# Kernel optimization log

Hardware: AMD Instinct MI355X
Metric: run time of the kernel (lower is better)

Reference implementation:

```python
import jax, jax.numpy as jnp
import numpy as np

N0, N1, N2, N3, B = 120000, 20000, 6000, 1600, 64
E1, E2, E3 = 480000, 144000, 38400
KS = 5  # kernel size per dim; K = 125 total


def spline_basis(pseudo, ks=KS):
    # open B-spline basis, degree 1, over [0,1]^3 (torch_spline_conv semantics)
    p = pseudo * (ks - 1)                       # (E,3)
    lo = jnp.clip(jnp.floor(p), 0.0, ks - 2.0)  # (E,3)
    f = p - lo                                  # fractional part
    bits = jnp.array([[(s >> d) & 1 for d in range(3)] for s in range(8)],
                     dtype=jnp.float32)         # (8,3) corner offsets
    w = jnp.where(bits[None] > 0, f[:, None, :], 1.0 - f[:, None, :])  # (E,8,3)
    basis = w[..., 0] * w[..., 1] * w[..., 2]   # (E,8)
    strides = jnp.array([1.0, ks, ks * ks], dtype=jnp.float32)
    kidx = ((lo[:, None, :] + bits[None]) * strides).sum(-1).astype(jnp.int32)  # (E,8)
    return basis, kidx


def spline_conv(x, edge_index, pseudo, W, root, bias, num_nodes):
    src, dst = edge_index[0], edge_index[1]
    basis, kidx = spline_basis(pseudo)                   # (E,8), (E,8)
    XW = jnp.einsum('ni,kio->nko', x, W)                 # (N,K,out)
    taps = XW[src[:, None], kidx]                        # (E,8,out) gather
    msg = (taps * basis[..., None]).sum(axis=1)          # (E,out)
    agg = jax.ops.segment_sum(msg, dst, num_segments=num_nodes)
    deg = jax.ops.segment_sum(jnp.ones_like(dst, jnp.float32), dst,
                              num_segments=num_nodes)
    agg = agg / jnp.maximum(deg, 1.0)[:, None]           # mean aggregation
    return agg + x @ root + bias


def seg_max(x, seg, n):
    v = jax.ops.segment_max(x, seg, num_segments=n)
    return jnp.where(jnp.isfinite(v), v, 0.0)  # empty voxels -> 0


def setup_inputs() -> dict:
    key = jax.random.key(0)
    ks = jax.random.split(key, 24)
    return {
        'x0': jax.random.uniform(ks[0], (N0, 1), jnp.float32),
        'cluster0': jax.random.randint(ks[1], (N0,), 0, N1),
        'edge1': jax.random.randint(ks[2], (2, E1), 0, N1),
        'pseudo1': jax.random.uniform(ks[3], (E1, 3), jnp.float32),
        'W1': jax.random.normal(ks[4], (125, 1, 64), jnp.float32) * 0.1,
        'root1': jax.random.normal(ks[5], (1, 64), jnp.float32) * 0.1,
        'b1': jnp.zeros((64,), jnp.float32),
        'cluster1': jax.random.randint(ks[6], (N1,), 0, N2),
        'edge2': jax.random.randint(ks[7], (2, E2), 0, N2),
        'pseudo2': jax.random.uniform(ks[8], (E2, 3), jnp.float32),
        'W2': jax.random.normal(ks[9], (125, 64, 64), jnp.float32) * 0.05,
        'root2': jax.random.normal(ks[10], (64, 64), jnp.float32) * 0.05,
        'b2': jnp.zeros((64,), jnp.float32),
        'cluster2': jax.random.randint(ks[11], (N2,), 0, N3),
        'edge3': jax.random.randint(ks[12], (2, E3), 0, N3),
        'pseudo3': jax.random.uniform(ks[13], (E3, 3), jnp.float32),
        'W3': jax.random.normal(ks[14], (125, 64, 128), jnp.float32) * 0.05,
        'root3': jax.random.normal(ks[15], (64, 128), jnp.float32) * 0.05,
        'b3': jnp.zeros((128,), jnp.float32),
        'cluster3': jax.random.randint(ks[16], (N3,), 0, B * 8),
        'fc1_w': jax.random.normal(ks[17], (1024, 256), jnp.float32) * 0.03,
        'fc1_b': jnp.zeros((256,), jnp.float32),
        'fc2_w': jax.random.normal(ks[18], (256, 10), jnp.float32) * 0.06,
        'fc2_b': jnp.zeros((10,), jnp.float32),
    }


def reference(x0, cluster0, edge1, pseudo1, W1, root1, b1,
              cluster1, edge2, pseudo2, W2, root2, b2,
              cluster2, edge3, pseudo3, W3, root3, b3,
              cluster3, fc1_w, fc1_b, fc2_w, fc2_b):
    x = seg_max(x0, cluster0, N1)                       # sparse voxel max pool 1
    x = jax.nn.elu(spline_conv(x, edge1, pseudo1, W1, root1, b1, N1))
    x = seg_max(x, cluster1, N2)                        # pool 2
    x = jax.nn.elu(spline_conv(x, edge2, pseudo2, W2, root2, b2, N2))
    x = seg_max(x, cluster2, N3)                        # pool 3
    x = jax.nn.elu(spline_conv(x, edge3, pseudo3, W3, root3, b3, N3))
    x = seg_max(x, cluster3, B * 8)                     # dense 2x2x2 voxel pool
    x = x.reshape(B, 8 * 128)
    x = jax.nn.elu(x @ fc1_w + fc1_b)
    x = x @ fc2_w + fc2_b
    return jax.nn.log_softmax(x, axis=1)
```

## Files before the change

### kernel.cpp

```cpp
#include <hip/hip_runtime.h>
#include <hip/hip_bf16.h>
#include <math.h>

#define N0c 120000
#define N1c 20000
#define N2c 6000
#define N3c 1600
#define E1c 480000
#define E2c 144000
#define E3c 38400

#define HB1 256
#define HB2 480
#define HB3 160
#define CVT2B 2000
#define CVT3B 4000
#define SS0B  469

typedef __attribute__((ext_vector_type(8))) short short8;
typedef __attribute__((ext_vector_type(4))) float f32x4;

__device__ __forceinline__ float eluf(float x) {
    return x > 0.0f ? x : expm1f(x);
}

__device__ __forceinline__ unsigned f2sort(float f) {
    unsigned u = __float_as_uint(f);
    return (u & 0x80000000u) ? ~u : (u | 0x80000000u);
}
__device__ __forceinline__ float sort2f(unsigned u) {
    unsigned bits = (u & 0x80000000u) ? (u & 0x7FFFFFFFu) : ~u;
    return __uint_as_float(bits);
}
__device__ __forceinline__ unsigned short f2bf(float v) {
    unsigned u = __float_as_uint(v);
    unsigned r = (u + 0x7FFFu + ((u >> 16) & 1u)) >> 16;
    return (unsigned short)r;
}

__global__ __launch_bounds__(256) void hist_all(
    const int* __restrict__ edge1, const int* __restrict__ edge2,
    const int* __restrict__ edge3,
    const float* __restrict__ pseudo2, const float* __restrict__ pseudo3,
    const float* __restrict__ W2, const float* __restrict__ W3,
    const float* __restrict__ x0, const int* __restrict__ cluster0,
    int* __restrict__ blockCnt1, int* __restrict__ binTot1,
    int* __restrict__ blockCnt2, int* __restrict__ binTot2, int* __restrict__ cntD2,
    int* __restrict__ blockCnt3, int* __restrict__ binTot3, int* __restrict__ cntD3,
    unsigned short* __restrict__ W2t, unsigned short* __restrict__ W3t,
    unsigned* __restrict__ xm1)
{
    __shared__ int h[1250];
    int b = blockIdx.x, t = threadIdx.x;
    if (b < HB1) {
        for (int i = t; i < 1250; i += 256) h[i] = 0;
        __syncthreads();
        for (int e = b * 256 + t; e < E1c; e += HB1 * 256)
            atomicAdd(&h[edge1[E1c + e] >> 4], 1);
        __syncthreads();
        for (int i = t; i < 1250; i += 256) {
            int v = h[i];
            blockCnt1[i * HB1 + b] = v;
            if (v) atomicAdd(&binTot1[i], v);
        }
    } else if (b < HB1 + HB2 + HB3) {
        bool is2 = b < HB1 + HB2;
        int rb = is2 ? (b - HB1) : (b - HB1 - HB2);
        int nblk = is2 ? HB2 : HB3;
        int E = is2 ? E2c : E3c;
        const int* edge = is2 ? edge2 : edge3;
        const float* pseudo = is2 ? pseudo2 : pseudo3;
        int* blockCnt = is2 ? blockCnt2 : blockCnt3;
        int* binTot = is2 ? binTot2 : binTot3;
        int* dstCnt = is2 ? cntD2 : cntD3;
        int nb = is2 ? HB2 : HB3;
        if (t < 64) h[t] = 0;
        __syncthreads();
        for (int e = rb * 256 + t; e < E; e += nblk * 256) {
            int c = 0, mul = 1;
            #pragma unroll
            for (int d = 0; d < 3; d++) {
                float p = pseudo[e * 3 + d] * 4.0f;
                float l = fminf(fmaxf(floorf(p), 0.0f), 3.0f);
                c += (int)l * mul;
                mul <<= 2;
            }
            atomicAdd(&h[c], 1);
            atomicAdd(&dstCnt[edge[E + e]], 1);
        }
        __syncthreads();
        if (t < 64) {
            int v = h[t];
            blockCnt[t * nb + rb] = v;
            if (v) atomicAdd(&binTot[t], v);
        }
    } else if (b < HB1 + HB2 + HB3 + CVT2B) {
        int idx = (b - (HB1 + HB2 + HB3)) * 256 + t;
        if (idx < 125 * 64 * 64) {
            int ic = idx & 63, kn = idx >> 6;
            int n = kn & 63, k = kn >> 6;
            W2t[idx] = f2bf(W2[((size_t)k * 64 + ic) * 64 + n]);
        }
    } else if (b < HB1 + HB2 + HB3 + CVT2B + CVT3B) {
        int idx = (b - (HB1 + HB2 + HB3 + CVT2B)) * 256 + t;
        if (idx < 125 * 128 * 64) {
            int ic = idx & 63, kn = idx >> 6;
            int n = kn & 127, k = kn >> 7;
            W3t[idx] = f2bf(W3[((size_t)k * 64 + ic) * 128 + n]);
        }
    } else {
        int idx = (b - (HB1 + HB2 + HB3 + CVT2B + CVT3B)) * 256 + t;
        if (idx < N0c)
            atomicMax(&xm1[cluster0[idx]], f2sort(x0[idx]));
    }
}

__global__ __launch_bounds__(256) void plan_tot(
    const int* __restrict__ binTot1, int* __restrict__ start1,
    const int* __restrict__ binTot2, int* __restrict__ binCnt2,
    int* __restrict__ binStart2, int* __restrict__ blkPrefix2,
    int* __restrict__ chunkBin2, int* __restrict__ chunkOff2,
    const int* __restrict__ binTot3, int* __restrict__ binCnt3,
    int* __restrict__ binStart3, int* __restrict__ blkPrefix3,
    int* __restrict__ chunkBin3, int* __restrict__ chunkOff3,
    const int* __restrict__ cntD2, int* __restrict__ dstStart2,
    const int* __restrict__ cntD3, int* __restrict__ dstStart3)
{
    __shared__ int ps[256];
    __shared__ int ps64[64];
    int t = threadIdx.x;

    int loc[5];
    int s = 0;
    #pragma unroll
    for (int i = 0; i < 5; i++) {
        int bin = t * 5 + i;
        int v = (bin < 1250) ? binTot1[bin] : 0;
        loc[i] = v;
        s += v;
    }
    ps[t] = s;
    __syncthreads();
    for (int ofs = 1; ofs < 256; ofs <<= 1) {
        int add = (t >= ofs) ? ps[t - ofs] : 0;
        __syncthreads();
        ps[t] += add;
        __syncthreads();
    }
    int run = (t == 0) ? 0 : ps[t - 1];
    #pragma unroll
    for (int i = 0; i < 5; i++) {
        int bin = t * 5 + i;
        if (bin < 1250) {
            start1[bin] = run;
            run += loc[i];
        }
    }
    if (t == 255) start1[1250] = run;
    __syncthreads();

    if (t < 64) {
        int v = binTot2[t];
        binCnt2[t] = v;
        ps64[t] = v;
    }
    __syncthreads();
    if (t == 0) {
        int s2 = 0, p = 0;
        for (int c = 0; c < 64; c++) {
            int v = ps64[c];
            binStart2[c] = s2;
            blkPrefix2[c] = p;
            s2 += v;
            p += (v + 63) >> 6;
        }
        binStart2[64] = s2;
        blkPrefix2[64] = p;
    }
    __syncthreads();
    if (t < 64) {
        int nch = (binCnt2[t] + 63) >> 6;
        int base = blkPrefix2[t];
        for (int j = 0; j < nch; j++) {
            chunkBin2[base + j] = t;
            chunkOff2[base + j] = j;
        }
    }
    __syncthreads();

    if (t < 64) {
        int v = binTot3[t];
        binCnt3[t] = v;
        ps64[t] = v;
    }
    __syncthreads();
    if (t == 0) {
        int s3 = 0, p = 0;
        for (int c = 0; c < 64; c++) {
            int v = ps64[c];
            binStart3[c] = s3;
            blkPrefix3[c] = p;
            s3 += v;
            p += (v + 63) >> 6;
        }
        binStart3[64] = s3;
        blkPrefix3[64] = p;
    }
    __syncthreads();
    if (t < 64) {
        int nch = (binCnt3[t] + 63) >> 6;
        int base = blkPrefix3[t];
        for (int j = 0; j < nch; j++) {
            chunkBin3[base + j] = t;
            chunkOff3[base + j] = j;
        }
    }
    __syncthreads();

    {
        int locd[24];
        int sd = 0;
        #pragma unroll
        for (int i = 0; i < 24; i++) {
            int bin = t * 24 + i;
            int vv = (bin < N2c) ? cntD2[bin] : 0;
            locd[i] = vv;
            sd += vv;
        }
        ps[t] = sd;
        __syncthreads();
        for (int ofs = 1; ofs < 256; ofs <<= 1) {
            int add = (t >= ofs) ? ps[t - ofs] : 0;
            __syncthreads();
            ps[t] += add;
            __syncthreads();
        }
        int rund = (t == 0) ? 0 : ps[t - 1];
        #pragma unroll
        for (int i = 0; i < 24; i++) {
            int bin = t * 24 + i;
            if (bin < N2c) { dstStart2[bin] = rund; rund += locd[i]; }
        }
        if (t == 255) dstStart2[N2c] = ps[255];
    }
    __syncthreads();

    {
        int locd[7];
        int sd = 0;
        #pragma unroll
        for (int i = 0; i < 7; i++) {
            int bin = t * 7 + i;
            int vv = (bin < N3c) ? cntD3[bin] : 0;
            locd[i] = vv;
            sd += vv;
        }
        ps[t] = sd;
        __syncthreads();
        for (int ofs = 1; ofs < 256; ofs <<= 1) {
            int add = (t >= ofs) ? ps[t - ofs] : 0;
            __syncthreads();
            ps[t] += add;
            __syncthreads();
        }
        int rund = (t == 0) ? 0 : ps[t - 1];
        #pragma unroll
        for (int i = 0; i < 7; i++) {
            int bin = t * 7 + i;
            if (bin < N3c) { dstStart3[bin] = rund; rund += locd[i]; }
        }
        if (t == 255) dstStart3[N3c] = ps[255];
    }
}

__global__ __launch_bounds__(256) void off_all(
    const int* __restrict__ blockCnt1, const int* __restrict__ start1,
    int* __restrict__ blockOff1,
    const int* __restrict__ blockCnt2, const int* __restrict__ binStart2,
    int* __restrict__ blockOff2,
    const int* __restrict__ blockCnt3, const int* __restrict__ binStart3,
    int* __restrict__ blockOff3)
{
    int wid = (blockIdx.x * 256 + threadIdx.x) >> 6;
    int lane = threadIdx.x & 63;
    if (wid >= 1250 + 64 + 64) return;
    const int* c;
    int* o;
    int run, width;
    if (wid < 1250) {
        c = blockCnt1 + (size_t)wid * HB1;
        o = blockOff1 + (size_t)wid * HB1;
        run = start1[wid];
        width = HB1;
    } else if (wid < 1250 + 64) {
        int bin = wid - 1250;
        c = blockCnt2 + (size_t)bin * HB2;
        o = blockOff2 + (size_t)bin * HB2;
        run = binStart2[bin];
        width = HB2;
    } else {
        int bin = wid - 1314;
        c = blockCnt3 + (size_t)bin * HB3;
        o = blockOff3 + (size_t)bin * HB3;
        run = binStart3[bin];
        width = HB3;
    }
    for (int base = 0; base < width; base += 64) {
        int b = base + lane;
        int v = (b < width) ? c[b] : 0;
        int inc = v;
        #pragma unroll
        for (int ofs = 1; ofs < 64; ofs <<= 1) {
            int u = __shfl_up(inc, ofs);
            if (lane >= ofs) inc += u;
        }
        if (b < width) o[b] = run + inc - v;
        run += __shfl(inc, 63);
    }
}

__global__ __launch_bounds__(256) void scatter_all(
    const int* __restrict__ edge1, const float* __restrict__ pseudo1,
    const int* __restrict__ edge2, const float* __restrict__ pseudo2,
    const int* __restrict__ edge3, const float* __restrict__ pseudo3,
    const int* __restrict__ blockOff1, const int* __restrict__ blockOff2,
    const int* __restrict__ blockOff3,
    int4* __restrict__ rec1, int4* __restrict__ rec2, int4* __restrict__ rec3,
    unsigned* __restrict__ xm1,
    const int* __restrict__ dstStart2, const int* __restrict__ dstStart3,
    int* __restrict__ curD2, int* __restrict__ curD3,
    int* __restrict__ posList2, int* __restrict__ posList3)
{
    __shared__ int cur[1250];
    int b = blockIdx.x, t = threadIdx.x;
    if (b < HB1) {
        for (int i = t; i < 1250; i += 256) cur[i] = blockOff1[(size_t)i * HB1 + b];
        __syncthreads();
        for (int e = b * 256 + t; e < E1c; e += HB1 * 256) {
            int src = edge1[e], dst = edge1[E1c + e];
            float f[3];
            int kbase = 0, mul5 = 1;
            #pragma unroll
            for (int d = 0; d < 3; d++) {
                float pp = pseudo1[e * 3 + d] * 4.0f;
                float l = fminf(fmaxf(floorf(pp), 0.0f), 3.0f);
                f[d] = pp - l;
                kbase += (int)l * mul5;
                mul5 *= 5;
            }
            int p = atomicAdd(&cur[dst >> 4], 1);
            rec1[p] = make_int4(src | ((dst & 15) << 16) | (kbase << 20),
                                __float_as_int(f[0]), __float_as_int(f[1]),
                                __float_as_int(f[2]));
        }
    } else if (b < HB1 + HB2 + HB3) {
        bool is2 = b < HB1 + HB2;
        int rb = is2 ? (b - HB1) : (b - HB1 - HB2);
        int nblk = is2 ? HB2 : HB3;
        int E = is2 ? E2c : E3c;
        const int* edge = is2 ? edge2 : edge3;
        const float* pseudo = is2 ? pseudo2 : pseudo3;
        const int* blockOff = is2 ? blockOff2 : blockOff3;
        int4* rec = is2 ? rec2 : rec3;
        const int* dstStart = is2 ? dstStart2 : dstStart3;
        int* curD = is2 ? curD2 : curD3;
        int* posList = is2 ? posList2 : posList3;
        int nb = is2 ? HB2 : HB3;
        if (t < 64) cur[t] = blockOff[(size_t)t * nb + rb];
        __syncthreads();
        for (int e = rb * 256 + t; e < E; e += nblk * 256) {
            int src = edge[e], dst = edge[E + e];
            float f[3];
            int c = 0, mul = 1;
            #pragma unroll
            for (int d = 0; d < 3; d++) {
                float pp = pseudo[e * 3 + d] * 4.0f;
                float l = fminf(fmaxf(floorf(pp), 0.0f), 3.0f);
                f[d] = pp - l;
                c += (int)l * mul;
                mul <<= 2;
            }
            int p = atomicAdd(&cur[c], 1);
            rec[p] = make_int4(src | (dst << 16),
                               __float_as_int(f[0]), __float_as_int(f[1]),
                               __float_as_int(f[2]));
            int qd = dstStart[dst] + atomicAdd(&curD[dst], 1);
            posList[qd] = p;
        }
    } else {
        int idx = (b - (HB1 + HB2 + HB3)) * 256 + t;
        if (idx < N1c) {
            float f = sort2f(xm1[idx]);
            unsigned bb = __float_as_uint(f);
            if ((bb & 0x7F800000u) == 0x7F800000u) f = 0.0f;
            ((float*)xm1)[idx] = f;
        }
    }
}

__global__ __launch_bounds__(256) void conv1_block(
    const int4* __restrict__ rec, const float* __restrict__ x,
    const int* __restrict__ start,
    const float* __restrict__ W, const float* __restrict__ root,
    const float* __restrict__ bias, const int* __restrict__ cl,
    unsigned* __restrict__ xmOut) {
    __shared__ float T[16][128];
    __shared__ int degL[16];
    int b = blockIdx.x;
    for (int j = threadIdx.x; j < 2048; j += 256) ((float*)T)[j] = 0.0f;
    if (threadIdx.x < 16) degL[threadIdx.x] = 0;
    __syncthreads();
    int s0 = start[b], s1 = start[b + 1];
    for (int i = s0 + threadIdx.x; i < s1; i += 256) {
        int4 r = rec[i];
        int src = r.x & 0xFFFF;
        int ln = (r.x >> 16) & 15;
        int kbase = r.x >> 20;
        float f0 = __int_as_float(r.y);
        float f1 = __int_as_float(r.z);
        float f2 = __int_as_float(r.w);
        float xv = x[src];
        #pragma unroll
        for (int s = 0; s < 8; s++) {
            int b0 = s & 1, b1 = (s >> 1) & 1, b2 = (s >> 2) & 1;
            float w0 = b0 ? f0 : 1.0f - f0;
            float w1 = b1 ? f1 : 1.0f - f1;
            float w2 = b2 ? f2 : 1.0f - f2;
            int k = kbase + b0 + 5 * b1 + 25 * b2;
            atomicAdd(&T[ln][k], xv * w0 * w1 * w2);
        }
        atomicAdd(&degL[ln], 1);
    }
    __syncthreads();
    int w = threadIdx.x >> 6, lane = threadIdx.x & 63;
    float acc[4] = {0.0f, 0.0f, 0.0f, 0.0f};
    for (int k = 0; k < 125; k++) {
        float wv = W[(k << 6) + lane];
        #pragma unroll
        for (int j = 0; j < 4; j++)
            acc[j] = fmaf(T[w + 4 * j][k], wv, acc[j]);
    }
    int v0 = b << 4;
    #pragma unroll
    for (int j = 0; j < 4; j++) {
        int ln = w + 4 * j;
        int v = v0 + ln;
        float d = fmaxf((float)degL[ln], 1.0f);
        float val = eluf(acc[j] / d + x[v] * root[lane] + bias[lane]);
        atomicMax(&xmOut[((size_t)cl[v] << 6) + lane], f2sort(val));
    }
}

__global__ void decode_cvt(unsigned* __restrict__ buf,
                           unsigned short* __restrict__ xb, int total) {
    int idx = blockIdx.x * blockDim.x + threadIdx.x;
    if (idx >= total) return;
    float f = sort2f(buf[idx]);
    unsigned b = __float_as_uint(f);
    if ((b & 0x7F800000u) == 0x7F800000u) f = 0.0f;
    ((float*)buf)[idx] = f;
    xb[idx] = f2bf(f);
}

__global__ void segmax_decode(unsigned* __restrict__ buf, int total) {
    int idx = blockIdx.x * blockDim.x + threadIdx.x;
    if (idx >= total) return;
    float f = sort2f(buf[idx]);
    unsigned b = __float_as_uint(f);
    if ((b & 0x7F800000u) == 0x7F800000u) f = 0.0f;
    ((float*)buf)[idx] = f;
}

template<int COUT>
__global__ __launch_bounds__(256) void spline_mfma(
    const int4* __restrict__ recs,
    const unsigned short* __restrict__ Wt,
    const unsigned short* __restrict__ xb,
    const int* __restrict__ binStart,
    const int* __restrict__ binCnt,
    const int* __restrict__ blkPrefix,
    const int* __restrict__ chunkBin,
    const int* __restrict__ chunkOff,
    float* __restrict__ msg)
{
    __shared__ float basisS[4][8][64];
    __shared__ int srcS[4][64];

    int w = threadIdx.x >> 6, lane = threadIdx.x & 63;
    int c = blockIdx.x * 4 + w;
    if (c >= blkPrefix[64]) return;
    int bin = chunkBin[c];
    int chunk = chunkOff[c];
    int cnt = binCnt[bin];

    {
        int pos = chunk * 64 + lane;
        bool act = pos < cnt;
        int4 r = act ? recs[binStart[bin] + pos] : make_int4(0, 0, 0, 0);
        srcS[w][lane] = r.x & 0xFFFF;
        float f0 = __int_as_float(r.y);
        float f1 = __int_as_float(r.z);
        float f2 = __int_as_float(r.w);
        #pragma unroll
        for (int s = 0; s < 8; s++) {
            float w0 = (s & 1) ? f0 : 1.0f - f0;
            float w1 = (s & 2) ? f1 : 1.0f - f1;
            float w2 = (s & 4) ? f2 : 1.0f - f2;
            basisS[w][s][lane] = act ? (w0 * w1 * w2) : 0.0f;
        }
    }
    __builtin_amdgcn_wave_barrier();
    __threadfence_block();

    int lo0 = bin & 3, lo1 = (bin >> 2) & 3, lo2 = bin >> 4;
    int kbase = lo0 + 5 * lo1 + 25 * lo2;
    int colOff = (COUT == 128) ? (blockIdx.y << 6) : 0;
    int q = lane >> 4;
    int mcol = lane & 15;

    short8 afr[4][2];
    #pragma unroll
    for (int rt = 0; rt < 4; rt++) {
        int src = srcS[w][rt * 16 + mcol];
        const unsigned short* xr = xb + ((size_t)src << 6) + q * 8;
        afr[rt][0] = *(const short8*)(xr);
        afr[rt][1] = *(const short8*)(xr + 32);
    }

    f32x4 acc[4][4];
    #pragma unroll
    for (int rt = 0; rt < 4; rt++)
        #pragma unroll
        for (int nt = 0; nt < 4; nt++)
            acc[rt][nt] = (f32x4){0.0f, 0.0f, 0.0f, 0.0f};
    const f32x4 zero4 = {0.0f, 0.0f, 0.0f, 0.0f};

    #pragma unroll 1
    for (int s = 0; s < 8; s++) {
        int k = kbase + (s & 1) + 5 * ((s >> 1) & 1) + 25 * (s >> 2);
        const unsigned short* Wk = Wt + ((size_t)k * COUT + colOff) * 64;
        short8 bfr[4][2];
        #pragma unroll
        for (int nt = 0; nt < 4; nt++) {
            const unsigned short* Wn = Wk + (size_t)(nt * 16 + mcol) * 64 + q * 8;
            bfr[nt][0] = *(const short8*)(Wn);
            bfr[nt][1] = *(const short8*)(Wn + 32);
        }
        #pragma unroll
        for (int rt = 0; rt < 4; rt++) {
            f32x4 ct[4];
            #pragma unroll
            for (int nt = 0; nt < 4; nt++) {
                ct[nt] = __builtin_amdgcn_mfma_f32_16x16x32_bf16(afr[rt][0], bfr[nt][0], zero4, 0, 0, 0);
                ct[nt] = __builtin_amdgcn_mfma_f32_16x16x32_bf16(afr[rt][1], bfr[nt][1], ct[nt], 0, 0, 0);
            }
            #pragma unroll
            for (int r = 0; r < 4; r++) {
                float bs = basisS[w][s][rt * 16 + q * 4 + r];
                #pragma unroll
                for (int nt = 0; nt < 4; nt++)
                    acc[rt][nt][r] = fmaf(bs, ct[nt][r], acc[rt][nt][r]);
            }
        }
    }

    int base = binStart[bin] + chunk * 64;
    #pragma unroll
    for (int rt = 0; rt < 4; rt++) {
        #pragma unroll
        for (int r = 0; r < 4; r++) {
            int row = rt * 16 + q * 4 + r;
            if (chunk * 64 + row < cnt) {
                float* mp = msg + (size_t)(base + row) * COUT + colOff + mcol;
                #pragma unroll
                for (int nt = 0; nt < 4; nt++)
                    mp[nt * 16] = acc[rt][nt][r];
            }
        }
    }
}

__global__ __launch_bounds__(256) void agg_update64(
    const float* __restrict__ msg, const int* __restrict__ posList,
    const int* __restrict__ dstStart,
    const float* __restrict__ xm, const float* __restrict__ root,
    const float* __restrict__ bias, const int* __restrict__ cl,
    unsigned* __restrict__ xmOut, int nNodes) {
    __shared__ float xsh[4][64];
    int w = threadIdx.x >> 6, lane = threadIdx.x & 63;
    int v = blockIdx.x * 4 + w;
    if (v >= nNodes) return;
    xsh[w][lane] = xm[((size_t)v << 6) + lane];
    int s0 = dstStart[v], s1 = dstStart[v + 1];
    float a0 = 0.0f, a1 = 0.0f, a2 = 0.0f, a3 = 0.0f;
    int i = s0;
    for (; i + 4 <= s1; i += 4) {
        int p0 = posList[i], p1 = posList[i + 1];
        int p2 = posList[i + 2], p3 = posList[i + 3];
        a0 += msg[((size_t)p0 << 6) + lane];
        a1 += msg[((size_t)p1 << 6) + lane];
        a2 += msg[((size_t)p2 << 6) + lane];
        a3 += msg[((size_t)p3 << 6) + lane];
    }
    for (; i < s1; i++)
        a0 += msg[((size_t)posList[i] << 6) + lane];
    float a = (a0 + a1 + a2 + a3) / fmaxf((float)(s1 - s0), 1.0f);
    float r = 0.0f;
    #pragma unroll 8
    for (int j = 0; j < 64; j++)
        r = fmaf(xsh[w][j], root[(j << 6) + lane], r);
    float val = eluf(a + r + bias[lane]);
    atomicMax(&xmOut[((size_t)cl[v] << 6) + lane], f2sort(val));
}

__global__ __launch_bounds__(256) void agg_update128(
    const float* __restrict__ msg, const int* __restrict__ posList,
    const int* __restrict__ dstStart,
    const float* __restrict__ xm, const float* __restrict__ root,
    const float* __restrict__ bias, const int* __restrict__ cl,
    unsigned* __restrict__ xmOut, int nNodes) {
    __shared__ float xsh[4][64];
    int w = threadIdx.x >> 6, lane = threadIdx.x & 63;
    int v = blockIdx.x * 4 + w;
    if (v >= nNodes) return;
    xsh[w][lane] = xm[((size_t)v << 6) + lane];
    int s0 = dstStart[v], s1 = dstStart[v + 1];
    float c0a = 0.0f, c0b = 0.0f, c1a = 0.0f, c1b = 0.0f;
    int i = s0;
    for (; i + 2 <= s1; i += 2) {
        int p0 = posList[i], p1 = posList[i + 1];
        const float* m0 = msg + ((size_t)p0 << 7);
        const float* m1 = msg + ((size_t)p1 << 7);
        c0a += m0[lane]; c0b += m0[64 + lane];
        c1a += m1[lane]; c1b += m1[64 + lane];
    }
    for (; i < s1; i++) {
        const float* m0 = msg + ((size_t)posList[i] << 7);
        c0a += m0[lane]; c0b += m0[64 + lane];
    }
    float dinv = 1.0f / fmaxf((float)(s1 - s0), 1.0f);
    float aa0 = (c0a + c1a) * dinv;
    float aa1 = (c0b + c1b) * dinv;
    float r0 = 0.0f, r1 = 0.0f;
    #pragma unroll 8
    for (int j = 0; j < 64; j++) {
        float xi = xsh[w][j];
        r0 = fmaf(xi, root[(j << 7) + lane], r0);
        r1 = fmaf(xi, root[(j << 7) + 64 + lane], r1);
    }
    unsigned* orow = xmOut + ((size_t)cl[v] << 7);
    atomicMax(&orow[lane], f2sort(eluf(aa0 + r0 + bias[lane])));
    atomicMax(&orow[64 + lane], f2sort(eluf(aa1 + r1 + bias[lane + 64])));
}

__global__ __launch_bounds__(256) void fc1_split(
    const float* __restrict__ xin, const float* __restrict__ w1,
    float* __restrict__ h) {
    __shared__ float xsh[128];
    int row = blockIdx.x, ks = blockIdx.y;
    int o = threadIdx.x;
    if (o < 128) xsh[o] = xin[row * 1024 + ks * 128 + o];
    __syncthreads();
    float acc = 0.0f;
    const float* wp = w1 + (size_t)ks * 128 * 256 + o;
    #pragma unroll 8
    for (int i = 0; i < 128; i++)
        acc = fmaf(xsh[i], wp[i * 256], acc);
    atomicAdd(&h[row * 256 + o], acc);
}

__global__ __launch_bounds__(64) void fc2_k(
    const float* __restrict__ h, const float* __restrict__ b1,
    const float* __restrict__ w2, const float* __restrict__ b2,
    float* __restrict__ out) {
    __shared__ float hs[256];
    __shared__ float lg[10];
    int row = blockIdx.x;
    int t = threadIdx.x;
    for (int i = t; i < 256; i += 64) hs[i] = eluf(h[row * 256 + i] + b1[i]);
    __syncthreads();
    if (t < 10) {
        float a = b2[t];
        for (int i = 0; i < 256; i++) a = fmaf(hs[i], w2[i * 10 + t], a);
        lg[t] = a;
    }
    __syncthreads();
    if (t < 10) {
        float m = -1e30f;
        #pragma unroll
        for (int j = 0; j < 10; j++) m = fmaxf(m, lg[j]);
        float sum = 0.0f;
        #pragma unroll
        for (int j = 0; j < 10; j++) sum += expf(lg[j] - m);
        out[row * 10 + t] = lg[t] - m - logf(sum);
    }
}

extern "C" void kernel_launch(void* const* d_in, const int* in_sizes, int n_in,
                              void* d_out, int out_size, void* d_ws, size_t ws_size,
                              hipStream_t stream) {
    const float* x0      = (const float*)d_in[0];
    const int*   cluster0= (const int*)d_in[1];
    const int*   edge1   = (const int*)d_in[2];
    const float* pseudo1 = (const float*)d_in[3];
    const float* W1      = (const float*)d_in[4];
    const float* root1   = (const float*)d_in[5];
    const float* b1      = (const float*)d_in[6];
    const int*   cluster1= (const int*)d_in[7];
    const int*   edge2   = (const int*)d_in[8];
    const float* pseudo2 = (const float*)d_in[9];
    const float* W2      = (const float*)d_in[10];
    const float* root2   = (const float*)d_in[11];
    const float* b2      = (const float*)d_in[12];
    const int*   cluster2= (const int*)d_in[13];
    const int*   edge3   = (const int*)d_in[14];
    const float* pseudo3 = (const float*)d_in[15];
    const float* W3      = (const float*)d_in[16];
    const float* root3   = (const float*)d_in[17];
    const float* b3      = (const float*)d_in[18];
    const int*   cluster3= (const int*)d_in[19];
    const float* fc1_w   = (const float*)d_in[20];
    const float* fc1_b   = (const float*)d_in[21];
    const float* fc2_w   = (const float*)d_in[22];
    const float* fc2_b   = (const float*)d_in[23];
    float* out = (float*)d_out;

    float* ws = (float*)d_ws;
    size_t off = 0;
    float* xm1  = ws + off; off += 20480;
    float* xm2  = ws + off; off += (size_t)N2c * 64;
    float* xm3  = ws + off; off += (size_t)N3c * 64;
    float* xm4  = ws + off; off += 512 * 128;
    float* h1   = ws + off; off += 64 * 256;
    int* cntD2   = (int*)(ws + off); off += 6016;
    int* cntD3   = (int*)(ws + off); off += 1664;
    int* curD2   = (int*)(ws + off); off += 6016;
    int* curD3   = (int*)(ws + off); off += 1664;
    int* binTot1 = (int*)(ws + off); off += 1280;
    int* binTot2 = (int*)(ws + off); off += 64;
    int* binTot3 = (int*)(ws + off); off += 64;
    size_t zeroFloats = off;
    int4* rec1 = (int4*)(ws + off); off += (size_t)E1c * 4;
    int4* rec2 = (int4*)(ws + off); off += (size_t)E2c * 4;
    int4* rec3 = (int4*)(ws + off); off += (size_t)E3c * 4;
    unsigned short* W2t = (unsigned short*)(ws + off); off += 256000;
    unsigned short* W3t = (unsigned short*)(ws + off); off += 512000;
    unsigned short* xb2 = (unsigned short*)(ws + off); off += 192000;
    unsigned short* xb3 = (unsigned short*)(ws + off); off += 51200;
    int* start1    = (int*)(ws + off); off += 1280;
    int* blockCnt1 = (int*)(ws + off); off += (size_t)HB1 * 1250;
    int* blockOff1 = (int*)(ws + off); off += (size_t)HB1 * 1250;
    int* blockCnt2 = (int*)(ws + off); off += (size_t)HB2 * 64;
    int* blockOff2 = (int*)(ws + off); off += (size_t)HB2 * 64;
    int* blockCnt3 = (int*)(ws + off); off += (size_t)HB3 * 64;
    int* blockOff3 = (int*)(ws + off); off += (size_t)HB3 * 64;
    int* binCnt2   = (int*)(ws + off); off += 64;
    int* binStart2 = (int*)(ws + off); off += 80;
    int* blkPrefix2= (int*)(ws + off); off += 80;
    int* chunkBin2 = (int*)(ws + off); off += 2560;
    int* chunkOff2 = (int*)(ws + off); off += 2560;
    int* binCnt3   = (int*)(ws + off); off += 64;
    int* binStart3 = (int*)(ws + off); off += 80;
    int* blkPrefix3= (int*)(ws + off); off += 80;
    int* chunkBin3 = (int*)(ws + off); off += 768;
    int* chunkOff3 = (int*)(ws + off); off += 768;
    int* dstStart2 = (int*)(ws + off); off += 6016;
    int* dstStart3 = (int*)(ws + off); off += 1664;
    int* posList2  = (int*)(ws + off); off += E2c;
    int* posList3  = (int*)(ws + off); off += E3c;
    float* msg = ws + off; off += (size_t)E2c * 64;

    hipMemsetAsync(d_ws, 0, zeroFloats * sizeof(float), stream);

    hist_all<<<HB1 + HB2 + HB3 + CVT2B + CVT3B + SS0B, 256, 0, stream>>>(
        edge1, edge2, edge3, pseudo2, pseudo3, W2, W3, x0, cluster0,
        blockCnt1, binTot1, blockCnt2, binTot2, cntD2,
        blockCnt3, binTot3, cntD3, W2t, W3t, (unsigned*)xm1);

    plan_tot<<<1, 256, 0, stream>>>(
        binTot1, start1,
        binTot2, binCnt2, binStart2, blkPrefix2, chunkBin2, chunkOff2,
        binTot3, binCnt3, binStart3, blkPrefix3, chunkBin3, chunkOff3,
        cntD2, dstStart2, cntD3, dstStart3);

    off_all<<<(1378 * 64 + 255) / 256, 256, 0, stream>>>(
        blockCnt1, start1, blockOff1,
        blockCnt2, binStart2, blockOff2,
        blockCnt3, binStart3, blockOff3);

    scatter_all<<<HB1 + HB2 + HB3 + (N1c + 255) / 256, 256, 0, stream>>>(
        edge1, pseudo1, edge2, pseudo2, edge3, pseudo3,
        blockOff1, blockOff2, blockOff3, rec1, rec2, rec3, (unsigned*)xm1,
        dstStart2, dstStart3, curD2, curD3, posList2, posList3);

    conv1_block<<<1250, 256, 0, stream>>>(rec1, xm1, start1, W1, root1, b1,
                                          cluster1, (unsigned*)xm2);
    decode_cvt<<<(N2c * 64) / 256, 256, 0, stream>>>((unsigned*)xm2, xb2, N2c * 64);

    spline_mfma<64><<<dim3((E2c / 64 + 64 + 3) / 4, 1), 256, 0, stream>>>(
        rec2, W2t, xb2, binStart2, binCnt2, blkPrefix2, chunkBin2, chunkOff2, msg);
    agg_update64<<<(N2c + 3) / 4, 256, 0, stream>>>(msg, posList2, dstStart2,
                                                    xm2, root2, b2, cluster2,
                                                    (unsigned*)xm3, N2c);
    decode_cvt<<<(N3c * 64) / 256, 256, 0, stream>>>((unsigned*)xm3, xb3, N3c * 64);

    spline_mfma<128><<<dim3((E3c / 64 + 64 + 3) / 4, 2), 256, 0, stream>>>(
        rec3, W3t, xb3, binStart3, binCnt3, blkPrefix3, chunkBin3, chunkOff3, msg);
    agg_update128<<<(N3c + 3) / 4, 256, 0, stream>>>(msg, posList3, dstStart3,
                                                     xm3, root3, b3, cluster3,
                                                     (unsigned*)xm4, N3c);
    segmax_decode<<<(512 * 128) / 256, 256, 0, stream>>>((unsigned*)xm4, 512 * 128);

    fc1_split<<<dim3(64, 8), 256, 0, stream>>>(xm4, fc1_w, h1);
    fc2_k<<<64, 64, 0, stream>>>(h1, fc1_b, fc2_w, fc2_b, out);
}
```

Baseline: 327.0 us.

## Use per-destination CSR for conv1, fp16 messages, LDS weight transpose, fuse decode

Conv1 edge bucketing moves from per-block 1250-bin histograms plus offset tables to a per-destination count, scan and atomic-cursor scatter, which removes the blockCnt1/blockOff1 traffic and their offset pass. The in-kernel degree count is replaced by dstStart differences. Weight transposition to bf16 now goes through a padded LDS tile per kernel index instead of thousands of strided-gather blocks. Edge messages between the MFMA and aggregation kernels are stored as fp16 rather than fp32, halving that traffic at some precision cost. The final seg-max decode is folded into fc1, removing one launch. The trade-off is that the conv1 scatter now uses global atomics per destination, which may contend more than the previous shared-memory bins.

```diff
diff --git a/kernel.cpp b/kernel.cpp
--- a/kernel.cpp
+++ b/kernel.cpp
@@ -1,5 +1,6 @@
 #include <hip/hip_runtime.h>
 #include <hip/hip_bf16.h>
+#include <hip/hip_fp16.h>
 #include <math.h>
 
 #define N0c 120000
@@ -13,8 +14,7 @@
 #define HB1 256
 #define HB2 480
 #define HB3 160
-#define CVT2B 2000
-#define CVT3B 4000
+#define WCVB 125
 #define SS0B  469
 
 typedef __attribute__((ext_vector_type(8))) short short8;
@@ -36,6 +36,12 @@
     unsigned u = __float_as_uint(v);
     unsigned r = (u + 0x7FFFu + ((u >> 16) & 1u)) >> 16;
     return (unsigned short)r;
+}
+__device__ __forceinline__ unsigned short f2h(float v) {
+    return __half_as_ushort(__float2half(v));
+}
+__device__ __forceinline__ float h2f(unsigned short u) {
+    return __half2float(__ushort_as_half(u));
 }
 
 __global__ __launch_bounds__(256) void hist_all(
@@ -44,25 +50,18 @@
     const float* __restrict__ pseudo2, const float* __restrict__ pseudo3,
     const float* __restrict__ W2, const float* __restrict__ W3,
     const float* __restrict__ x0, const int* __restrict__ cluster0,
-    int* __restrict__ blockCnt1, int* __restrict__ binTot1,
+    int* __restrict__ cntD1,
     int* __restrict__ blockCnt2, int* __restrict__ binTot2, int* __restrict__ cntD2,
     int* __restrict__ blockCnt3, int* __restrict__ binTot3, int* __restrict__ cntD3,
     unsigned short* __restrict__ W2t, unsigned short* __restrict__ W3t,
     unsigned* __restrict__ xm1)
 {
-    __shared__ int h[1250];
+    __shared__ float smf[64 * 129];
+    int* h = (int*)smf;
     int b = blockIdx.x, t = threadIdx.x;
     if (b < HB1) {
-        for (int i = t; i < 1250; i += 256) h[i] = 0;
-        __syncthreads();
         for (int e = b * 256 + t; e < E1c; e += HB1 * 256)
-            atomicAdd(&h[edge1[E1c + e] >> 4], 1);
-        __syncthreads();
-        for (int i = t; i < 1250; i += 256) {
-            int v = h[i];
-            blockCnt1[i * HB1 + b] = v;
-            if (v) atomicAdd(&binTot1[i], v);
-        }
+            atomicAdd(&cntD1[edge1[E1c + e]], 1);
     } else if (b < HB1 + HB2 + HB3) {
         bool is2 = b < HB1 + HB2;
         int rb = is2 ? (b - HB1) : (b - HB1 - HB2);
@@ -94,29 +93,37 @@
             blockCnt[t * nb + rb] = v;
             if (v) atomicAdd(&binTot[t], v);
         }
-    } else if (b < HB1 + HB2 + HB3 + CVT2B) {
-        int idx = (b - (HB1 + HB2 + HB3)) * 256 + t;
-        if (idx < 125 * 64 * 64) {
-            int ic = idx & 63, kn = idx >> 6;
-            int n = kn & 63, k = kn >> 6;
-            W2t[idx] = f2bf(W2[((size_t)k * 64 + ic) * 64 + n]);
-        }
-    } else if (b < HB1 + HB2 + HB3 + CVT2B + CVT3B) {
-        int idx = (b - (HB1 + HB2 + HB3 + CVT2B)) * 256 + t;
-        if (idx < 125 * 128 * 64) {
-            int ic = idx & 63, kn = idx >> 6;
-            int n = kn & 127, k = kn >> 7;
-            W3t[idx] = f2bf(W3[((size_t)k * 64 + ic) * 128 + n]);
+    } else if (b < HB1 + HB2 + HB3 + WCVB) {
+        int k = b - (HB1 + HB2 + HB3);
+        for (int idx = t; idx < 4096; idx += 256) {
+            int n = idx & 63, ic = idx >> 6;
+            smf[ic * 65 + n] = W2[((size_t)k * 64 + ic) * 64 + n];
+        }
+        __syncthreads();
+        for (int idx = t; idx < 4096; idx += 256) {
+            int ic = idx & 63, n = idx >> 6;
+            W2t[((size_t)k * 64 + n) * 64 + ic] = f2bf(smf[ic * 65 + n]);
+        }
+    } else if (b < HB1 + HB2 + HB3 + 2 * WCVB) {
+        int k = b - (HB1 + HB2 + HB3 + WCVB);
+        for (int idx = t; idx < 8192; idx += 256) {
+            int n = idx & 127, ic = idx >> 7;
+            smf[ic * 129 + n] = W3[((size_t)k * 64 + ic) * 128 + n];
+        }
+        __syncthreads();
+        for (int idx = t; idx < 8192; idx += 256) {
+            int ic = idx & 63, n = idx >> 6;
+            W3t[((size_t)k * 128 + n) * 64 + ic] = f2bf(smf[ic * 129 + n]);
         }
     } else {
-        int idx = (b - (HB1 + HB2 + HB3 + CVT2B + CVT3B)) * 256 + t;
+        int idx = (b - (HB1 + HB2 + HB3 + 2 * WCVB)) * 256 + t;
         if (idx < N0c)
             atomicMax(&xm1[cluster0[idx]], f2sort(x0[idx]));
     }
 }
 
 __global__ __launch_bounds__(256) void plan_tot(
-    const int* __restrict__ binTot1, int* __restrict__ start1,
+    const int* __restrict__ cntD1, int* __restrict__ dstStart1,
     const int* __restrict__ binTot2, int* __restrict__ binCnt2,
     int* __restrict__ binStart2, int* __restrict__ blkPrefix2,
     int* __restrict__ chunkBin2, int* __restrict__ chunkOff2,
@@ -130,33 +137,23 @@
     __shared__ int ps64[64];
     int t = threadIdx.x;
 
-    int loc[5];
-    int s = 0;
-    #pragma unroll
-    for (int i = 0; i < 5; i++) {
-        int bin = t * 5 + i;
-        int v = (bin < 1250) ? binTot1[bin] : 0;
-        loc[i] = v;
-        s += v;
-    }
-    ps[t] = s;
-    __syncthreads();
-    for (int ofs = 1; ofs < 256; ofs <<= 1) {
-        int add = (t >= ofs) ? ps[t - ofs] : 0;
+    {
+        int a0 = t * 79;
+        int a1 = min(a0 + 79, N1c);
+        int sum = 0;
+        for (int bin = a0; bin < a1; bin++) sum += cntD1[bin];
+        ps[t] = sum;
         __syncthreads();
-        ps[t] += add;
-        __syncthreads();
-    }
-    int run = (t == 0) ? 0 : ps[t - 1];
-    #pragma unroll
-    for (int i = 0; i < 5; i++) {
-        int bin = t * 5 + i;
-        if (bin < 1250) {
-            start1[bin] = run;
-            run += loc[i];
-        }
-    }
-    if (t == 255) start1[1250] = run;
+        for (int ofs = 1; ofs < 256; ofs <<= 1) {
+            int add = (t >= ofs) ? ps[t - ofs] : 0;
+            __syncthreads();
+            ps[t] += add;
+            __syncthreads();
+        }
+        int run = (t == 0) ? 0 : ps[t - 1];
+        for (int bin = a0; bin < a1; bin++) { dstStart1[bin] = run; run += cntD1[bin]; }
+        if (t == 255) dstStart1[N1c] = ps[255];
+    }
     __syncthreads();
 
     if (t < 64) {
@@ -274,8 +271,6 @@
 }
 
 __global__ __launch_bounds__(256) void off_all(
-    const int* __restrict__ blockCnt1, const int* __restrict__ start1,
-    int* __restrict__ blockOff1,
     const int* __restrict__ blockCnt2, const int* __restrict__ binStart2,
     int* __restrict__ blockOff2,
     const int* __restrict__ blockCnt3, const int* __restrict__ binStart3,
@@ -283,23 +278,17 @@
 {
     int wid = (blockIdx.x * 256 + threadIdx.x) >> 6;
     int lane = threadIdx.x & 63;
-    if (wid >= 1250 + 64 + 64) return;
+    if (wid >= 128) return;
     const int* c;
     int* o;
     int run, width;
-    if (wid < 1250) {
-        c = blockCnt1 + (size_t)wid * HB1;
-        o = blockOff1 + (size_t)wid * HB1;
-        run = start1[wid];
-        width = HB1;
-    } else if (wid < 1250 + 64) {
-        int bin = wid - 1250;
-        c = blockCnt2 + (size_t)bin * HB2;
-        o = blockOff2 + (size_t)bin * HB2;
-        run = binStart2[bin];
+    if (wid < 64) {
+        c = blockCnt2 + (size_t)wid * HB2;
+        o = blockOff2 + (size_t)wid * HB2;
+        run = binStart2[wid];
         width = HB2;
     } else {
-        int bin = wid - 1314;
+        int bin = wid - 64;
         c = blockCnt3 + (size_t)bin * HB3;
         o = blockOff3 + (size_t)bin * HB3;
         run = binStart3[bin];
@@ -323,19 +312,17 @@
     const int* __restrict__ edge1, const float* __restrict__ pseudo1,
     const int* __restrict__ edge2, const float* __restrict__ pseudo2,
     const int* __restrict__ edge3, const float* __restrict__ pseudo3,
-    const int* __restrict__ blockOff1, const int* __restrict__ blockOff2,
-    const int* __restrict__ blockOff3,
+    const int* __restrict__ dstStart1, int* __restrict__ curD1,
+    const int* __restrict__ blockOff2, const int* __restrict__ blockOff3,
     int4* __restrict__ rec1, int4* __restrict__ rec2, int4* __restrict__ rec3,
     unsigned* __restrict__ xm1,
     const int* __restrict__ dstStart2, const int* __restrict__ dstStart3,
     int* __restrict__ curD2, int* __restrict__ curD3,
     int* __restrict__ posList2, int* __restrict__ posList3)
 {
-    __shared__ int cur[1250];
+    __shared__ int cur[64];
     int b = blockIdx.x, t = threadIdx.x;
     if (b < HB1) {
-        for (int i = t; i < 1250; i += 256) cur[i] = blockOff1[(size_t)i * HB1 + b];
-        __syncthreads();
         for (int e = b * 256 + t; e < E1c; e += HB1 * 256) {
             int src = edge1[e], dst = edge1[E1c + e];
             float f[3];
@@ -348,7 +335,7 @@
                 kbase += (int)l * mul5;
                 mul5 *= 5;
             }
-            int p = atomicAdd(&cur[dst >> 4], 1);
+            int p = dstStart1[dst] + atomicAdd(&curD1[dst], 1);
             rec1[p] = make_int4(src | ((dst & 15) << 16) | (kbase << 20),
                                 __float_as_int(f[0]), __float_as_int(f[1]),
                                 __float_as_int(f[2]));
@@ -400,17 +387,16 @@
 
 __global__ __launch_bounds__(256) void conv1_block(
     const int4* __restrict__ rec, const float* __restrict__ x,
-    const int* __restrict__ start,
+    const int* __restrict__ dstStart1,
     const float* __restrict__ W, const float* __restrict__ root,
     const float* __restrict__ bias, const int* __restrict__ cl,
     unsigned* __restrict__ xmOut) {
     __shared__ float T[16][128];
-    __shared__ int degL[16];
     int b = blockIdx.x;
     for (int j = threadIdx.x; j < 2048; j += 256) ((float*)T)[j] = 0.0f;
-    if (threadIdx.x < 16) degL[threadIdx.x] = 0;
-    __syncthreads();
-    int s0 = start[b], s1 = start[b + 1];
+    __syncthreads();
+    int v0 = b << 4;
+    int s0 = dstStart1[v0], s1 = dstStart1[v0 + 16];
     for (int i = s0 + threadIdx.x; i < s1; i += 256) {
         int4 r = rec[i];
         int src = r.x & 0xFFFF;
@@ -429,7 +415,6 @@
             int k = kbase + b0 + 5 * b1 + 25 * b2;
             atomicAdd(&T[ln][k], xv * w0 * w1 * w2);
         }
-        atomicAdd(&degL[ln], 1);
     }
     __syncthreads();
     int w = threadIdx.x >> 6, lane = threadIdx.x & 63;
@@ -440,12 +425,11 @@
         for (int j = 0; j < 4; j++)
             acc[j] = fmaf(T[w + 4 * j][k], wv, acc[j]);
     }
-    int v0 = b << 4;
     #pragma unroll
     for (int j = 0; j < 4; j++) {
         int ln = w + 4 * j;
         int v = v0 + ln;
-        float d = fmaxf((float)degL[ln], 1.0f);
+        float d = fmaxf((float)(dstStart1[v + 1] - dstStart1[v]), 1.0f);
         float val = eluf(acc[j] / d + x[v] * root[lane] + bias[lane]);
         atomicMax(&xmOut[((size_t)cl[v] << 6) + lane], f2sort(val));
     }
@@ -460,15 +444,6 @@
     if ((b & 0x7F800000u) == 0x7F800000u) f = 0.0f;
     ((float*)buf)[idx] = f;
     xb[idx] = f2bf(f);
-}
-
-__global__ void segmax_decode(unsigned* __restrict__ buf, int total) {
-    int idx = blockIdx.x * blockDim.x + threadIdx.x;
-    if (idx >= total) return;
-    float f = sort2f(buf[idx]);
-    unsigned b = __float_as_uint(f);
-    if ((b & 0x7F800000u) == 0x7F800000u) f = 0.0f;
-    ((float*)buf)[idx] = f;
 }
 
 template<int COUT>
@@ -481,7 +456,7 @@
     const int* __restrict__ blkPrefix,
     const int* __restrict__ chunkBin,
     const int* __restrict__ chunkOff,
-    float* __restrict__ msg)
+    unsigned short* __restrict__ msg)
 {
     __shared__ float basisS[4][8][64];
     __shared__ int srcS[4][64];
@@ -571,17 +546,17 @@
         for (int r = 0; r < 4; r++) {
             int row = rt * 16 + q * 4 + r;
             if (chunk * 64 + row < cnt) {
-                float* mp = msg + (size_t)(base + row) * COUT + colOff + mcol;
+                unsigned short* mp = msg + (size_t)(base + row) * COUT + colOff + mcol;
                 #pragma unroll
                 for (int nt = 0; nt < 4; nt++)
-                    mp[nt * 16] = acc[rt][nt][r];
+                    mp[nt * 16] = f2h(acc[rt][nt][r]);
             }
         }
     }
 }
 
 __global__ __launch_bounds__(256) void agg_update64(
-    const float* __restrict__ msg, const int* __restrict__ posList,
+    const unsigned short* __restrict__ msg, const int* __restrict__ posList,
     const int* __restrict__ dstStart,
     const float* __restrict__ xm, const float* __restrict__ root,
     const float* __restrict__ bias, const int* __restrict__ cl,
@@ -597,13 +572,13 @@
     for (; i + 4 <= s1; i += 4) {
         int p0 = posList[i], p1 = posList[i + 1];
         int p2 = posList[i + 2], p3 = posList[i + 3];
-        a0 += msg[((size_t)p0 << 6) + lane];
-        a1 += msg[((size_t)p1 << 6) + lane];
-        a2 += msg[((size_t)p2 << 6) + lane];
-        a3 += msg[((size_t)p3 << 6) + lane];
+        a0 += h2f(msg[((size_t)p0 << 6) + lane]);
+        a1 += h2f(msg[((size_t)p1 << 6) + lane]);
+        a2 += h2f(msg[((size_t)p2 << 6) + lane]);
+        a3 += h2f(msg[((size_t)p3 << 6) + lane]);
     }
     for (; i < s1; i++)
-        a0 += msg[((size_t)posList[i] << 6) + lane];
+        a0 += h2f(msg[((size_t)posList[i] << 6) + lane]);
     float a = (a0 + a1 + a2 + a3) / fmaxf((float)(s1 - s0), 1.0f);
     float r = 0.0f;
     #pragma unroll 8
@@ -614,7 +589,7 @@
 }
 
 __global__ __launch_bounds__(256) void agg_update128(
-    const float* __restrict__ msg, const int* __restrict__ posList,
+    const unsigned short* __restrict__ msg, const int* __restrict__ posList,
     const int* __restrict__ dstStart,
     const float* __restrict__ xm, const float* __restrict__ root,
     const float* __restrict__ bias, const int* __restrict__ cl,
@@ -629,14 +604,14 @@
     int i = s0;
     for (; i + 2 <= s1; i += 2) {
         int p0 = posList[i], p1 = posList[i + 1];
-        const float* m0 = msg + ((size_t)p0 << 7);
-        const float* m1 = msg + ((size_t)p1 << 7);
-        c0a += m0[lane]; c0b += m0[64 + lane];
-        c1a += m1[lane]; c1b += m1[64 + lane];
+        const unsigned short* m0 = msg + ((size_t)p0 << 7);
+        const unsigned short* m1 = msg + ((size_t)p1 << 7);
+        c0a += h2f(m0[lane]); c0b += h2f(m0[64 + lane]);
+        c1a += h2f(m1[lane]); c1b += h2f(m1[64 + lane]);
     }
     for (; i < s1; i++) {
-        const float* m0 = msg + ((size_t)posList[i] << 7);
-        c0a += m0[lane]; c0b += m0[64 + lane];
+        const unsigned short* m0 = msg + ((size_t)posList[i] << 7);
+        c0a += h2f(m0[lane]); c0b += h2f(m0[64 + lane]);
     }
     float dinv = 1.0f / fmaxf((float)(s1 - s0), 1.0f);
     float aa0 = (c0a + c1a) * dinv;
@@ -654,12 +629,17 @@
 }
 
 __global__ __launch_bounds__(256) void fc1_split(
-    const float* __restrict__ xin, const float* __restrict__ w1,
+    const unsigned* __restrict__ xin, const float* __restrict__ w1,
     float* __restrict__ h) {
     __shared__ float xsh[128];
     int row = blockIdx.x, ks = blockIdx.y;
     int o = threadIdx.x;
-    if (o < 128) xsh[o] = xin[row * 1024 + ks * 128 + o];
+    if (o < 128) {
+        float f = sort2f(xin[row * 1024 + ks * 128 + o]);
+        unsigned bb = __float_as_uint(f);
+        if ((bb & 0x7F800000u) == 0x7F800000u) f = 0.0f;
+        xsh[o] = f;
+    }
     __syncthreads();
     float acc = 0.0f;
     const float* wp = w1 + (size_t)ks * 128 * 256 + o;
@@ -732,11 +712,12 @@
     float* xm3  = ws + off; off += (size_t)N3c * 64;
     float* xm4  = ws + off; off += 512 * 128;
     float* h1   = ws + off; off += 64 * 256;
+    int* cntD1   = (int*)(ws + off); off += 20032;
+    int* curD1   = (int*)(ws + off); off += 20032;
     int* cntD2   = (int*)(ws + off); off += 6016;
     int* cntD3   = (int*)(ws + off); off += 1664;
     int* curD2   = (int*)(ws + off); off += 6016;
     int* curD3   = (int*)(ws + off); off += 1664;
-    int* binTot1 = (int*)(ws + off); off += 1280;
     int* binTot2 = (int*)(ws + off); off += 64;
     int* binTot3 = (int*)(ws + off); off += 64;
     size_t zeroFloats = off;
@@ -747,9 +728,7 @@
     unsigned short* W3t = (unsigned short*)(ws + off); off += 512000;
     unsigned short* xb2 = (unsigned short*)(ws + off); off += 192000;
     unsigned short* xb3 = (unsigned short*)(ws + off); off += 51200;
-    int* start1    = (int*)(ws + off); off += 1280;
-    int* blockCnt1 = (int*)(ws + off); off += (size_t)HB1 * 1250;
-    int* blockOff1 = (int*)(ws + off); off += (size_t)HB1 * 1250;
+    int* dstStart1 = (int*)(ws + off); off += 20032;
     int* blockCnt2 = (int*)(ws + off); off += (size_t)HB2 * 64;
     int* blockOff2 = (int*)(ws + off); off += (size_t)HB2 * 64;
     int* blockCnt3 = (int*)(ws + off); off += (size_t)HB3 * 64;
@@ -768,32 +747,31 @@
     int* dstStart3 = (int*)(ws + off); off += 1664;
     int* posList2  = (int*)(ws + off); off += E2c;
     int* posList3  = (int*)(ws + off); off += E3c;
-    float* msg = ws + off; off += (size_t)E2c * 64;
+    unsigned short* msg = (unsigned short*)(ws + off); off += (size_t)E2c * 32;
 
     hipMemsetAsync(d_ws, 0, zeroFloats * sizeof(float), stream);
 
-    hist_all<<<HB1 + HB2 + HB3 + CVT2B + CVT3B + SS0B, 256, 0, stream>>>(
+    hist_all<<<HB1 + HB2 + HB3 + 2 * WCVB + SS0B, 256, 0, stream>>>(
         edge1, edge2, edge3, pseudo2, pseudo3, W2, W3, x0, cluster0,
-        blockCnt1, binTot1, blockCnt2, binTot2, cntD2,
+        cntD1, blockCnt2, binTot2, cntD2,
         blockCnt3, binTot3, cntD3, W2t, W3t, (unsigned*)xm1);
 
     plan_tot<<<1, 256, 0, stream>>>(
-        binTot1, start1,
+        cntD1, dstStart1,
         binTot2, binCnt2, binStart2, blkPrefix2, chunkBin2, chunkOff2,
         binTot3, binCnt3, binStart3, blkPrefix3, chunkBin3, chunkOff3,
         cntD2, dstStart2, cntD3, dstStart3);
 
-    off_all<<<(1378 * 64 + 255) / 256, 256, 0, stream>>>(
-        blockCnt1, start1, blockOff1,
+    off_all<<<32, 256, 0, stream>>>(
         blockCnt2, binStart2, blockOff2,
         blockCnt3, binStart3, blockOff3);
 
     scatter_all<<<HB1 + HB2 + HB3 + (N1c + 255) / 256, 256, 0, stream>>>(
         edge1, pseudo1, edge2, pseudo2, edge3, pseudo3,
-        blockOff1, blockOff2, blockOff3, rec1, rec2, rec3, (unsigned*)xm1,
+        dstStart1, curD1, blockOff2, blockOff3, rec1, rec2, rec3, (unsigned*)xm1,
         dstStart2, dstStart3, curD2, curD3, posList2, posList3);
 
-    conv1_block<<<1250, 256, 0, stream>>>(rec1, xm1, start1, W1, root1, b1,
+    conv1_block<<<1250, 256, 0, stream>>>(rec1, xm1, dstStart1, W1, root1, b1,
                                           cluster1, (unsigned*)xm2);
     decode_cvt<<<(N2c * 64) / 256, 256, 0, stream>>>((unsigned*)xm2, xb2, N2c * 64);
 
@@ -809,8 +787,7 @@
     agg_update128<<<(N3c + 3) / 4, 256, 0, stream>>>(msg, posList3, dstStart3,
                                                      xm3, root3, b3, cluster3,
                                                      (unsigned*)xm4, N3c);
-    segmax_decode<<<(512 * 128) / 256, 256, 0, stream>>>((unsigned*)xm4, 512 * 128);
-
-    fc1_split<<<dim3(64, 8), 256, 0, stream>>>(xm4, fc1_w, h1);
+
+    fc1_split<<<dim3(64, 8), 256, 0, stream>>>((unsigned*)xm4, fc1_w, h1);
     fc2_k<<<64, 64, 0, stream>>>(h1, fc1_b, fc2_w, fc2_b, out);
 }
```

Measured after the change: 383.9 us. +17.4%, slower.
